# Kernel tuning notes

Measured on AMD Instinct MI355X. Metric: run time of the kernel, lower is better.

## Reference

```python
import jax, jax.numpy as jnp
import numpy as np

B, S, D, H = 2, 2048, 1024, 16
DEPTH = D // H


def setup_inputs() -> dict:
    key = jax.random.key(0)
    ks = jax.random.split(key, 6)
    q = jax.random.normal(ks[0], (B, S, D), dtype=jnp.float32)
    k = jax.random.normal(ks[1], (B, S, D), dtype=jnp.float32)
    v = jax.random.normal(ks[2], (B, S, D), dtype=jnp.float32)
    # causal mask, broadcastable to [B, H, S, S]
    mask = jnp.tril(jnp.ones((S, S), dtype=bool))[None, None, :, :]
    wq = jax.random.normal(ks[3], (D, D), dtype=jnp.float32)
    wk = jax.random.normal(ks[4], (D, D), dtype=jnp.float32)
    wv = jax.random.normal(ks[5], (D, D), dtype=jnp.float32)
    return {"q": q, "k": k, "v": v, "mask": mask, "wq": wq, "wk": wk, "wv": wv}


def _split_heads(x):
    # [B, S, D] -> [B, H, S, depth]
    return x.reshape(x.shape[0], -1, H, DEPTH).transpose(0, 2, 1, 3)


def reference(q, k, v, mask, wq, wk, wv):
    q = _split_heads(q @ wq)
    k = _split_heads(k @ wk)
    v = _split_heads(v @ wv)
    scale = jnp.sqrt(jnp.float32(DEPTH))
    # [B, H, S, S]
    scores = jnp.einsum("bhqd,bhkd->bhqk", q, k) / scale
    scores = jnp.where(mask, scores, jnp.float32(-8.0))
    scores = scores - jnp.max(scores, axis=-1, keepdims=True)
    attn = jax.nn.softmax(scores, axis=-1)
    out = jnp.einsum("bhqk,bhkd->bhqd", attn, v)
    # [B, H, S, depth] -> [B, S, D]
    return out.transpose(0, 2, 1, 3).reshape(out.shape[0], -1, D)
```

## Files before the change

kernel.cpp:

```cpp
#include <hip/hip_runtime.h>
#include <hip/hip_bf16.h>

#define B_  2
#define S_  2048
#define D_  1024
#define H_  16
#define DH_ 64

typedef __attribute__((ext_vector_type(8)))  short  short8;
typedef __attribute__((ext_vector_type(4)))  short  short4b;
typedef __attribute__((ext_vector_type(16))) float  f32x16;

#define MFMA32(A,B,C) __builtin_amdgcn_mfma_f32_32x32x16_bf16(A,B,C,0,0,0)

static __device__ __forceinline__ short bf16b(float x) {
    __hip_bfloat16 h = __float2bfloat16(x);
    return *(short*)&h;
}
static __device__ __forceinline__ float bf16tof(short s) {
    union { unsigned u; float f; } cv;
    cv.u = ((unsigned)(unsigned short)s) << 16;
    return cv.f;
}
static __device__ __forceinline__ void gl2lds(const short* g, short* l) {
    __builtin_amdgcn_global_load_lds(
        (const __attribute__((address_space(1))) unsigned int*)g,
        (__attribute__((address_space(3))) unsigned int*)l, 16, 0, 0);
}
static __device__ __forceinline__ unsigned cvtpk(float a, float b) {
    unsigned r;
    asm("v_cvt_pk_bf16_f32 %0, %1, %2" : "=v"(r) : "v"(a), "v"(b));
    return r;
}
static __device__ __forceinline__ void pl32swap(unsigned &a, unsigned &b) {
    asm volatile("v_permlane32_swap_b32 %0, %1" : "+v"(a), "+v"(b));
}

__global__ __launch_bounds__(256)
void conv_x(const float* __restrict__ q, const float* __restrict__ k,
            const float* __restrict__ v, char* __restrict__ ws) {
    const int z = blockIdx.y;
    const float* src = z == 0 ? q : z == 1 ? k : v;
    short* hi = (short*)(ws + (size_t)z * 16777216);
    short* lo = hi + 4194304;
    const int i = (blockIdx.x * 256 + threadIdx.x) * 4;
    float4 xv = *(const float4*)&src[i];
    const float* xf = (const float*)&xv;
    short4b h4, l4;
#pragma unroll
    for (int e = 0; e < 4; ++e) {
        short hb = bf16b(xf[e]);
        h4[e] = hb;
        l4[e] = bf16b(xf[e] - bf16tof(hb));
    }
    *(short4b*)&hi[i] = h4;
    *(short4b*)&lo[i] = l4;
}

__global__ __launch_bounds__(256)
void conv_wT(const float* __restrict__ wq, const float* __restrict__ wk,
             const float* __restrict__ wv, char* __restrict__ ws) {
    __shared__ short HiT[64][80];
    __shared__ short LoT[64][80];
    const int z = blockIdx.z;
    const float* w = z == 0 ? wq : z == 1 ? wk : wv;
    short* oh = (short*)(ws + 50331648 + (size_t)z * 4194304);
    short* ol = oh + 1048576;
    const int t  = threadIdx.x;
    const int k0 = blockIdx.x * 64, n0 = blockIdx.y * 64;

    const int kr = t >> 2, c4 = (t & 3) * 16;
    const float* srow = w + (size_t)(k0 + kr) * 1024 + n0 + c4;
#pragma unroll
    for (int u = 0; u < 16; u += 4) {
        float4 f = *(const float4*)&srow[u];
        const float* ff = (const float*)&f;
#pragma unroll
        for (int e = 0; e < 4; ++e) {
            int nl = c4 + u + e;
            short hb = bf16b(ff[e]);
            HiT[nl][kr] = hb;
            LoT[nl][kr] = bf16b(ff[e] - bf16tof(hb));
        }
    }
    __syncthreads();
    const int nl = t >> 2, kc = (t & 3) * 16;
    size_t off = (size_t)(n0 + nl) * 1024 + k0 + kc;
    *(short8*)&oh[off]     = *(const short8*)&HiT[nl][kc];
    *(short8*)&oh[off + 8] = *(const short8*)&HiT[nl][kc + 8];
    *(short8*)&ol[off]     = *(const short8*)&LoT[nl][kc];
    *(short8*)&ol[off + 8] = *(const short8*)&LoT[nl][kc + 8];
}

#define AHI_ 0
#define ALO_ 4096
#define BHI_ 8192
#define BLO_ 12288

__global__ __launch_bounds__(256, 2)
void proj_mfma(const short* __restrict__ xh0, const short* __restrict__ xl0,
               const short* __restrict__ xh1, const short* __restrict__ xl1,
               const short* __restrict__ xh2, const short* __restrict__ xl2,
               const short* __restrict__ wh0, const short* __restrict__ wl0,
               const short* __restrict__ wh1, const short* __restrict__ wl1,
               const short* __restrict__ wh2, const short* __restrict__ wl2,
               short* __restrict__ qh, short* __restrict__ ql,
               short* __restrict__ kh, short* __restrict__ kl,
               short* __restrict__ vt) {
    __shared__ __align__(16) short lds[32768];
    const int z  = blockIdx.z;
    const int m0 = blockIdx.y * 128;
    const int n0 = blockIdx.x * 128;
    const int t = threadIdx.x, lane = t & 63, w = t >> 6;
    const int l31 = lane & 31, hh = lane >> 5;

    const short* xh = z == 0 ? xh0 : z == 1 ? xh1 : xh2;
    const short* xl = z == 0 ? xl0 : z == 1 ? xl1 : xl2;
    const short* wh = z == 0 ? wh0 : z == 1 ? wh1 : wh2;
    const short* wl = z == 0 ? wl0 : z == 1 ? wl1 : wl2;

    const short* gsrc[8];
    short*       ldst[8];
#pragma unroll
    for (int j = 0; j < 8; ++j) {
        int sub = ((j & 1) << 2) | w;
        int cc  = (sub << 6) | lane;
        int row = cc >> 2, p = cc & 3;
        int kc  = p ^ ((row & 3) ^ ((row >> 2) & 3));
        bool isA  = j < 4;
        bool isHi = (j & 2) == 0;
        const short* base = isA ? (isHi ? xh : xl) : (isHi ? wh : wl);
        int r0g = isA ? m0 : n0;
        gsrc[j] = base + (size_t)(r0g + row) * 1024 + kc * 8;
        ldst[j] = &lds[(j >> 1) * 4096 + sub * 512];
    }

    const int rm0 = ((w & 1) << 6) + l31, rm1 = rm0 + 32;
    const int rn0 = ((w >> 1) << 6) + l31, rn1 = rn0 + 32;
    const int swm = (rm0 & 3) ^ ((rm0 >> 2) & 3);
    const int swn = (rn0 & 3) ^ ((rn0 >> 2) & 3);

    f32x16 accs[2][2] = {};

#pragma unroll
    for (int j = 0; j < 8; ++j)
        gl2lds(gsrc[j], ldst[j]);

    for (int kt = 0; kt < 32; ++kt) {
        const int cb = (kt & 1) << 14;
        if (kt < 31) {
            const int nb = 16384 - cb;
#pragma unroll
            for (int j = 0; j < 8; ++j)
                gl2lds(gsrc[j] + (kt + 1) * 32, ldst[j] + nb);
            asm volatile("s_waitcnt vmcnt(8)" ::: "memory");
        } else {
            asm volatile("s_waitcnt vmcnt(0)" ::: "memory");
        }
        __builtin_amdgcn_s_barrier();
        __builtin_amdgcn_sched_barrier(0);
        __builtin_amdgcn_s_setprio(1);
#pragma unroll
        for (int ks = 0; ks < 2; ++ks) {
            const int kc = (ks << 1) | hh;
            const int om = ((kc ^ swm) << 3) + cb;
            const int on = ((kc ^ swn) << 3) + cb;
            short8 ah0 = *(const short8*)&lds[AHI_ + rm0 * 32 + om];
            short8 ah1 = *(const short8*)&lds[AHI_ + rm1 * 32 + om];
            short8 al0 = *(const short8*)&lds[ALO_ + rm0 * 32 + om];
            short8 al1 = *(const short8*)&lds[ALO_ + rm1 * 32 + om];
            short8 bh0 = *(const short8*)&lds[BHI_ + rn0 * 32 + on];
            short8 bh1 = *(const short8*)&lds[BHI_ + rn1 * 32 + on];
            short8 bl0 = *(const short8*)&lds[BLO_ + rn0 * 32 + on];
            short8 bl1 = *(const short8*)&lds[BLO_ + rn1 * 32 + on];
            accs[0][0] = MFMA32(ah0, bh0, accs[0][0]);
            accs[0][1] = MFMA32(ah0, bh1, accs[0][1]);
            accs[1][0] = MFMA32(ah1, bh0, accs[1][0]);
            accs[1][1] = MFMA32(ah1, bh1, accs[1][1]);
            accs[0][0] = MFMA32(ah0, bl0, accs[0][0]);
            accs[0][1] = MFMA32(ah0, bl1, accs[0][1]);
            accs[1][0] = MFMA32(ah1, bl0, accs[1][0]);
            accs[1][1] = MFMA32(ah1, bl1, accs[1][1]);
            accs[0][0] = MFMA32(al0, bh0, accs[0][0]);
            accs[0][1] = MFMA32(al0, bh1, accs[0][1]);
            accs[1][0] = MFMA32(al1, bh0, accs[1][0]);
            accs[1][1] = MFMA32(al1, bh1, accs[1][1]);
        }
        __builtin_amdgcn_s_setprio(0);
        __builtin_amdgcn_sched_barrier(0);
        __builtin_amdgcn_s_barrier();
    }

    const int qm = w & 1, qn = w >> 1;
    const int bb = m0 >> 11;
    const int sbase = (m0 & 2047) + qm * 64;
    if (z < 2) {
        short* oh = z == 0 ? qh : kh;
        short* ol = z == 0 ? ql : kl;
#pragma unroll
        for (int mt = 0; mt < 2; ++mt)
#pragma unroll
        for (int nt = 0; nt < 2; ++nt) {
            int n_g = n0 + qn * 64 + nt * 32 + l31;
            int h = n_g >> 6, d = n_g & 63;
#pragma unroll
            for (int r = 0; r < 16; ++r) {
                int s = sbase + mt * 32 + (r & 3) + 8 * (r >> 2) + 4 * hh;
                size_t off = (((size_t)(bb * 16 + h) * 2048 + s) << 6) + d;
                float a = accs[mt][nt][r];
                short hb = bf16b(a);
                oh[off] = hb;
                ol[off] = bf16b(a - bf16tof(hb));
            }
        }
    } else {
#pragma unroll
        for (int mt = 0; mt < 2; ++mt)
#pragma unroll
        for (int nt = 0; nt < 2; ++nt) {
            int n_g = n0 + qn * 64 + nt * 32 + l31;
            int h = n_g >> 6, d = n_g & 63;
            size_t vbase = ((size_t)(bb * 16 + h) * 64 + d) * 2048;
#pragma unroll
            for (int r2 = 0; r2 < 4; ++r2) {
                int s0 = sbase + mt * 32 + 8 * r2 + 4 * hh;
                short4b pk;
#pragma unroll
                for (int a2 = 0; a2 < 4; ++a2)
                    pk[a2] = bf16b(accs[mt][nt][r2 * 4 + a2]);
                *(short4b*)&vt[vbase + s0] = pk;
            }
        }
    }
}

__global__ __launch_bounds__(256)
void vsums(const short* __restrict__ Vt, float* __restrict__ SV) {
    __shared__ float TSl[32][64];
    const int bh = blockIdx.x;
    const int d = threadIdx.x & 63, g = threadIdx.x >> 6;
    const short* row = Vt + ((size_t)bh * DH_ + d) * S_;
#pragma unroll
    for (int ci = 0; ci < 8; ++ci) {
        int c = g * 8 + ci;
        float s = 0.f;
#pragma unroll
        for (int j = 0; j < 8; ++j) {
            short8 v = *(const short8*)&row[c * 64 + j * 8];
#pragma unroll
            for (int e = 0; e < 8; ++e) s += bf16tof(v[e]);
        }
        TSl[c][d] = s;
    }
    __syncthreads();
    if (threadIdx.x < 64) {
        float run = 0.f;
#pragma unroll
        for (int c = 32; c >= 0; --c) {
            SV[((size_t)bh * 33 + c) * 64 + d] = run;
            if (c > 0) run += TSl[c - 1][d];
        }
    }
}

__global__ __launch_bounds__(256, 2)
void attn_mfma(const short* __restrict__ Qhi, const short* __restrict__ Qlo,
               const short* __restrict__ Khi, const short* __restrict__ Klo,
               const short* __restrict__ Vt,  const float* __restrict__ SV,
               float* __restrict__ out) {
    __shared__ __align__(16) short SBUF[24576];
#define KhiS (SBUF)
#define KloS (SBUF + 8192)
#define VtS  (SBUF + 16384)

    const int t     = threadIdx.x;
    const int lane  = t & 63;
    const int w     = t >> 6;
    const int l31   = lane & 31;
    const int hh    = lane >> 5;
    const int bh    = blockIdx.x;
    const int yy    = blockIdx.y;
    const int qt    = (yy < 8) ? yy : 23 - yy;
    const int q0    = qt * 128;
    const int myq   = q0 + w * 32 + l31;
    const int ktend = 2 * qt + 2;

    const size_t basebh = (size_t)bh * S_ * DH_;

    short8 qh[4], ql[4];
    {
        const short* qr = Qhi + basebh + (size_t)myq * DH_;
        const short* lr = Qlo + basebh + (size_t)myq * DH_;
#pragma unroll
        for (int kf = 0; kf < 4; ++kf) {
            int dofs = kf * 16 + hh * 8;
            qh[kf] = *(const short8*)(qr + dofs);
            ql[kf] = *(const short8*)(lr + dofs);
        }
    }

    const int i1 = (w << 6) | lane;
    const int i2 = 256 + i1;
    const int r1 = i1 >> 3, c1 = (i1 & 7) ^ (r1 & 7);
    const int r2 = i2 >> 3, c2 = (i2 & 7) ^ (r2 & 7);
    const short* gKh1 = Khi + basebh + (size_t)r1 * 64 + c1 * 8;
    const short* gKh2 = Khi + basebh + (size_t)r2 * 64 + c2 * 8;
    const short* gKl1 = Klo + basebh + (size_t)r1 * 64 + c1 * 8;
    const short* gKl2 = Klo + basebh + (size_t)r2 * 64 + c2 * 8;
    const short* gV1  = Vt  + basebh + (size_t)r1 * S_ + c1 * 8;
    const short* gV2  = Vt  + basebh + (size_t)r2 * S_ + c2 * 8;
    const int wub = w << 9;

#define ASTAGE(KT, BUF) do {                                                  \
        const int ka_ = (KT) * 4096, va_ = (KT) * 64, bo_ = (BUF) * 4096;     \
        gl2lds(gKh1 + ka_, &KhiS[bo_ + wub]);                                 \
        gl2lds(gKh2 + ka_, &KhiS[bo_ + 2048 + wub]);                          \
        gl2lds(gKl1 + ka_, &KloS[bo_ + wub]);                                 \
        gl2lds(gKl2 + ka_, &KloS[bo_ + 2048 + wub]);                          \
        gl2lds(gV1  + va_, &VtS [bo_ + wub]);                                 \
        gl2lds(gV2  + va_, &VtS [bo_ + 2048 + wub]);                          \
    } while (0)

    float m_run = -INFINITY, l_run = 0.f;
    f32x16 oT0 = {}, oT1 = {};

    const int sw0 = l31 & 7;

    ASTAGE(0, 0);

    for (int kt = 0; kt < ktend; ++kt) {
        const int bo = (kt & 1) << 12;
        if (kt + 1 < ktend) {
            ASTAGE(kt + 1, (kt & 1) ^ 1);
            asm volatile("s_waitcnt vmcnt(6)" ::: "memory");
        } else {
            asm volatile("s_waitcnt vmcnt(0)" ::: "memory");
        }
        __builtin_amdgcn_s_barrier();
        __builtin_amdgcn_sched_barrier(0);

        f32x16 acc0 = {}, acc1 = {};
        __builtin_amdgcn_s_setprio(1);
#pragma unroll
        for (int kf = 0; kf < 4; ++kf) {
            const int cs = ((2 * kf + hh) ^ sw0) << 3;
            short8 k0h = *(const short8*)&KhiS[bo + l31 * 64 + cs];
            short8 k0l = *(const short8*)&KloS[bo + l31 * 64 + cs];
            short8 k1h = *(const short8*)&KhiS[bo + (l31 + 32) * 64 + cs];
            short8 k1l = *(const short8*)&KloS[bo + (l31 + 32) * 64 + cs];
            acc0 = MFMA32(k0h, qh[kf], acc0);
            acc0 = MFMA32(k0h, ql[kf], acc0);
            acc0 = MFMA32(k0l, qh[kf], acc0);
            acc1 = MFMA32(k1h, qh[kf], acc1);
            acc1 = MFMA32(k1h, ql[kf], acc1);
            acc1 = MFMA32(k1l, qh[kf], acc1);
        }
        __builtin_amdgcn_s_setprio(0);

        float vals[32];
        float tmax = -INFINITY;
#pragma unroll
        for (int r = 0; r < 16; ++r) {
            int key0 = kt * 64 + ((r & 3) + 8 * (r >> 2) + 4 * hh);
            float v0 = acc0[r] * 0.125f;
            v0 = (key0 <= myq) ? v0 : -8.0f;
            float v1 = acc1[r] * 0.125f;
            v1 = (key0 + 32 <= myq) ? v1 : -8.0f;
            vals[r] = v0;
            vals[16 + r] = v1;
            tmax = fmaxf(tmax, fmaxf(v0, v1));
        }
        tmax = fmaxf(tmax, __shfl_xor(tmax, 32, 64));
        const bool defer = __all(tmax <= m_run + 8.0f);
        if (!defer) {
            float mnew  = fmaxf(m_run, tmax);
            float alpha = __expf(m_run - mnew);
            l_run *= alpha;
#pragma unroll
            for (int r = 0; r < 16; ++r) { oT0[r] *= alpha; oT1[r] *= alpha; }
            m_run = mnew;
        }
        float psum = 0.f;
        unsigned cw[16];
#pragma unroll
        for (int tt = 0; tt < 16; ++tt) {
            float p0 = __expf(vals[2 * tt]     - m_run);
            float p1 = __expf(vals[2 * tt + 1] - m_run);
            psum += p0 + p1;
            cw[tt] = cvtpk(p0, p1);
        }
        psum += __shfl_xor(psum, 32, 64);
        l_run += psum;

        __builtin_amdgcn_s_setprio(1);
#pragma unroll
        for (int kf = 0; kf < 4; ++kf) {
            unsigned w0 = cw[4 * kf],     w1 = cw[4 * kf + 1];
            unsigned w2 = cw[4 * kf + 2], w3 = cw[4 * kf + 3];
            pl32swap(w0, w2);
            pl32swap(w1, w3);
            union { unsigned u[4]; short8 s8; } pu;
            pu.u[0] = w0; pu.u[1] = w1; pu.u[2] = w2; pu.u[3] = w3;
            const int cs = ((2 * kf + hh) ^ sw0) << 3;
            short8 v0 = *(const short8*)&VtS[bo + l31 * 64 + cs];
            short8 v1 = *(const short8*)&VtS[bo + (l31 + 32) * 64 + cs];
            oT0 = MFMA32(v0, pu.s8, oT0);
            oT1 = MFMA32(v1, pu.s8, oT1);
        }
        __builtin_amdgcn_s_setprio(0);
        __builtin_amdgcn_sched_barrier(0);
        __builtin_amdgcn_s_barrier();
    }
#undef ASTAGE

    {
        float mfin = fmaxf(m_run, -8.0f);
        float aa   = __expf(m_run - mfin);
        float e8   = __expf(-8.0f - mfin);
        float nrem = (float)(S_ - ktend * 64);
        float lfin = l_run * aa + nrem * e8;
        float inv  = 1.0f / lfin;
        const float* sv = SV + ((size_t)bh * 33 + ktend) * 64;
#pragma unroll
        for (int r = 0; r < 16; ++r) {
            int dim0 = (r & 3) + 8 * (r >> 2) + 4 * hh;
            oT0[r] = (oT0[r] * aa + e8 * sv[dim0])      * inv;
            oT1[r] = (oT1[r] * aa + e8 * sv[dim0 + 32]) * inv;
        }
    }

    __syncthreads();
    float* Ob = (float*)SBUF + w * 2176;
#pragma unroll
    for (int r = 0; r < 16; ++r) {
        int dim0 = (r & 3) + 8 * (r >> 2) + 4 * hh;
        Ob[l31 * 68 + dim0]      = oT0[r];
        Ob[l31 * 68 + dim0 + 32] = oT1[r];
    }
    {
        const int qq = lane >> 1;
        const int ch = (lane & 1) * 32;
        const float* src = Ob + qq * 68 + ch;
        const int b  = bh >> 4;
        const int h  = bh & 15;
        float* dst = out + ((size_t)b * S_ + (q0 + w * 32 + qq)) * D_ + h * 64 + ch;
#pragma unroll
        for (int c = 0; c < 32; c += 4)
            *(float4*)(dst + c) = *(const float4*)(src + c);
    }
#undef KhiS
#undef KloS
#undef VtS
}

extern "C" void kernel_launch(void* const* d_in, const int* in_sizes, int n_in,
                              void* d_out, int out_size, void* d_ws, size_t ws_size,
                              hipStream_t stream) {
    const float* q  = (const float*)d_in[0];
    const float* k  = (const float*)d_in[1];
    const float* v  = (const float*)d_in[2];
    const float* wq = (const float*)d_in[4];
    const float* wk = (const float*)d_in[5];
    const float* wv = (const float*)d_in[6];
    float* out = (float*)d_out;

    char* ws = (char*)d_ws;
    const short* XH[3] = {(short*)ws, (short*)(ws + 16777216), (short*)(ws + 33554432)};
    const short* XL[3] = {XH[0] + 4194304, XH[1] + 4194304, XH[2] + 4194304};
    const short* WH[3] = {(short*)(ws + 50331648), (short*)(ws + 54525952), (short*)(ws + 58720256)};
    const short* WL[3] = {WH[0] + 1048576, WH[1] + 1048576, WH[2] + 1048576};
    float* SV = (float*)(ws + 62914560 + 262144);

    short *Qhi, *Qlo, *Khi, *Klo, *Vt;
    if (ws_size >= (size_t)109051904) {
        Qhi = (short*)(ws + 67108864);
        Qlo = (short*)(ws + 75497472);
        Khi = (short*)(ws + 83886080);
        Klo = (short*)(ws + 92274688);
        Vt  = (short*)(ws + 100663296);
    } else {
        Qhi = (short*)d_in[0]; Qlo = Qhi + 4194304;
        Khi = (short*)d_in[1]; Klo = Khi + 4194304;
        Vt  = (short*)d_in[2];
    }

    conv_x <<<dim3(4096, 3), 256, 0, stream>>>(q, k, v, ws);
    conv_wT<<<dim3(16, 16, 3), 256, 0, stream>>>(wq, wk, wv, ws);

    proj_mfma<<<dim3(8, 32, 3), 256, 0, stream>>>(
        XH[0], XL[0], XH[1], XL[1], XH[2], XL[2],
        WH[0], WL[0], WH[1], WL[1], WH[2], WL[2],
        Qhi, Qlo, Khi, Klo, Vt);

    vsums<<<32, 256, 0, stream>>>(Vt, SV);

    attn_mfma<<<dim3(32, 16), 256, 0, stream>>>(Qhi, Qlo, Khi, Klo, Vt, SV, out);
}
```

Measured before the change: 280.8 us.

## Merge conversion kernels and fold V suffix sums into attention kernel

Combines the activation and weight bf16 hi/lo conversion kernels into one launch that picks its role from a flattened block index. It also drops the separate vsums kernel: each attention block now sums the masked-out tail of V for its query tile directly into shared memory before the main loop. This cuts two kernel launches and the SV round-trip through global memory. In exchange, every attention block reads its V tail redundantly (up to the full sequence for early tiles), which adds global traffic and latency at kernel start.

```diff
diff --git a/kernel.cpp b/kernel.cpp
--- a/kernel.cpp
+++ b/kernel.cpp
@@ -37,37 +37,41 @@
 }
 
 __global__ __launch_bounds__(256)
-void conv_x(const float* __restrict__ q, const float* __restrict__ k,
-            const float* __restrict__ v, char* __restrict__ ws) {
-    const int z = blockIdx.y;
-    const float* src = z == 0 ? q : z == 1 ? k : v;
-    short* hi = (short*)(ws + (size_t)z * 16777216);
-    short* lo = hi + 4194304;
-    const int i = (blockIdx.x * 256 + threadIdx.x) * 4;
-    float4 xv = *(const float4*)&src[i];
-    const float* xf = (const float*)&xv;
-    short4b h4, l4;
-#pragma unroll
-    for (int e = 0; e < 4; ++e) {
-        short hb = bf16b(xf[e]);
-        h4[e] = hb;
-        l4[e] = bf16b(xf[e] - bf16tof(hb));
-    }
-    *(short4b*)&hi[i] = h4;
-    *(short4b*)&lo[i] = l4;
-}
-
-__global__ __launch_bounds__(256)
-void conv_wT(const float* __restrict__ wq, const float* __restrict__ wk,
-             const float* __restrict__ wv, char* __restrict__ ws) {
+void conv_all(const float* __restrict__ q, const float* __restrict__ k,
+              const float* __restrict__ v,
+              const float* __restrict__ wq, const float* __restrict__ wk,
+              const float* __restrict__ wv, char* __restrict__ ws) {
     __shared__ short HiT[64][80];
     __shared__ short LoT[64][80];
-    const int z = blockIdx.z;
+    const int bid = blockIdx.x;
+    const int t   = threadIdx.x;
+    if (bid < 12288) {
+        const int z   = bid >> 12;
+        const int xb  = bid & 4095;
+        const float* src = z == 0 ? q : z == 1 ? k : v;
+        short* hi = (short*)(ws + (size_t)z * 16777216);
+        short* lo = hi + 4194304;
+        const int i = (xb * 256 + t) * 4;
+        float4 xv = *(const float4*)&src[i];
+        const float* xf = (const float*)&xv;
+        short4b h4, l4;
+#pragma unroll
+        for (int e = 0; e < 4; ++e) {
+            short hb = bf16b(xf[e]);
+            h4[e] = hb;
+            l4[e] = bf16b(xf[e] - bf16tof(hb));
+        }
+        *(short4b*)&hi[i] = h4;
+        *(short4b*)&lo[i] = l4;
+        return;
+    }
+    const int wid = bid - 12288;
+    const int z   = wid >> 8;
+    const int rem = wid & 255;
+    const int k0  = (rem & 15) << 6, n0 = (rem >> 4) << 6;
     const float* w = z == 0 ? wq : z == 1 ? wk : wv;
     short* oh = (short*)(ws + 50331648 + (size_t)z * 4194304);
     short* ol = oh + 1048576;
-    const int t  = threadIdx.x;
-    const int k0 = blockIdx.x * 64, n0 = blockIdx.y * 64;
 
     const int kr = t >> 2, c4 = (t & 3) * 16;
     const float* srow = w + (size_t)(k0 + kr) * 1024 + n0 + c4;
@@ -234,41 +238,13 @@
     }
 }
 
-__global__ __launch_bounds__(256)
-void vsums(const short* __restrict__ Vt, float* __restrict__ SV) {
-    __shared__ float TSl[32][64];
-    const int bh = blockIdx.x;
-    const int d = threadIdx.x & 63, g = threadIdx.x >> 6;
-    const short* row = Vt + ((size_t)bh * DH_ + d) * S_;
-#pragma unroll
-    for (int ci = 0; ci < 8; ++ci) {
-        int c = g * 8 + ci;
-        float s = 0.f;
-#pragma unroll
-        for (int j = 0; j < 8; ++j) {
-            short8 v = *(const short8*)&row[c * 64 + j * 8];
-#pragma unroll
-            for (int e = 0; e < 8; ++e) s += bf16tof(v[e]);
-        }
-        TSl[c][d] = s;
-    }
-    __syncthreads();
-    if (threadIdx.x < 64) {
-        float run = 0.f;
-#pragma unroll
-        for (int c = 32; c >= 0; --c) {
-            SV[((size_t)bh * 33 + c) * 64 + d] = run;
-            if (c > 0) run += TSl[c - 1][d];
-        }
-    }
-}
-
 __global__ __launch_bounds__(256, 2)
 void attn_mfma(const short* __restrict__ Qhi, const short* __restrict__ Qlo,
                const short* __restrict__ Khi, const short* __restrict__ Klo,
-               const short* __restrict__ Vt,  const float* __restrict__ SV,
-               float* __restrict__ out) {
+               const short* __restrict__ Vt,  float* __restrict__ out) {
     __shared__ __align__(16) short SBUF[24576];
+    __shared__ float svp[4][64];
+    __shared__ float svs[64];
 #define KhiS (SBUF)
 #define KloS (SBUF + 8192)
 #define VtS  (SBUF + 16384)
@@ -286,6 +262,21 @@
     const int ktend = 2 * qt + 2;
 
     const size_t basebh = (size_t)bh * S_ * DH_;
+
+    {
+        const int s_begin = ktend * 64;
+        float part = 0.f;
+        const short* vrow = Vt + basebh + (size_t)lane * S_;
+        for (int s = s_begin + w * 8; s < S_; s += 32) {
+            short8 vv = *(const short8*)&vrow[s];
+#pragma unroll
+            for (int e = 0; e < 8; ++e) part += bf16tof(vv[e]);
+        }
+        svp[w][lane] = part;
+    }
+    __syncthreads();
+    if (t < 64)
+        svs[t] = svp[0][t] + svp[1][t] + svp[2][t] + svp[3][t];
 
     short8 qh[4], ql[4];
     {
@@ -420,12 +411,11 @@
         float nrem = (float)(S_ - ktend * 64);
         float lfin = l_run * aa + nrem * e8;
         float inv  = 1.0f / lfin;
-        const float* sv = SV + ((size_t)bh * 33 + ktend) * 64;
 #pragma unroll
         for (int r = 0; r < 16; ++r) {
             int dim0 = (r & 3) + 8 * (r >> 2) + 4 * hh;
-            oT0[r] = (oT0[r] * aa + e8 * sv[dim0])      * inv;
-            oT1[r] = (oT1[r] * aa + e8 * sv[dim0 + 32]) * inv;
+            oT0[r] = (oT0[r] * aa + e8 * svs[dim0])      * inv;
+            oT1[r] = (oT1[r] * aa + e8 * svs[dim0 + 32]) * inv;
         }
     }
 
@@ -469,7 +459,6 @@
     const short* XL[3] = {XH[0] + 4194304, XH[1] + 4194304, XH[2] + 4194304};
     const short* WH[3] = {(short*)(ws + 50331648), (short*)(ws + 54525952), (short*)(ws + 58720256)};
     const short* WL[3] = {WH[0] + 1048576, WH[1] + 1048576, WH[2] + 1048576};
-    float* SV = (float*)(ws + 62914560 + 262144);
 
     short *Qhi, *Qlo, *Khi, *Klo, *Vt;
     if (ws_size >= (size_t)109051904) {
@@ -484,15 +473,12 @@
         Vt  = (short*)d_in[2];
     }
 
-    conv_x <<<dim3(4096, 3), 256, 0, stream>>>(q, k, v, ws);
-    conv_wT<<<dim3(16, 16, 3), 256, 0, stream>>>(wq, wk, wv, ws);
+    conv_all<<<dim3(13056), 256, 0, stream>>>(q, k, v, wq, wk, wv, ws);
 
     proj_mfma<<<dim3(8, 32, 3), 256, 0, stream>>>(
         XH[0], XL[0], XH[1], XL[1], XH[2], XL[2],
         WH[0], WL[0], WH[1], WL[1], WH[2], WL[2],
         Qhi, Qlo, Khi, Klo, Vt);
 
-    vsums<<<32, 256, 0, stream>>>(Vt, SV);
-
-    attn_mfma<<<dim3(32, 16), 256, 0, stream>>>(Qhi, Qlo, Khi, Klo, Vt, SV, out);
-}
+    attn_mfma<<<dim3(32, 16), 256, 0, stream>>>(Qhi, Qlo, Khi, Klo, Vt, out);
+}
```

Result: faster. 273.3 us (-2.7%).
